# Kernel tuning notes

Hardware: AMD Instinct MI355X
Metric: run time of the kernel (lower is better)

The kernel has to match this reference:

```python
import jax, jax.numpy as jnp
import numpy as np

N_NODES = 50000
N_EDGES = 1000000
D_IN = 64
D_OUT = 64
N_REL = 8


def setup_inputs() -> dict:
    key = jax.random.key(0)
    ks = jax.random.split(key, 8)
    x = jax.random.normal(ks[0], (N_NODES, D_IN), dtype=jnp.float32)
    edge_src = jax.random.randint(ks[1], (N_EDGES,), 0, N_NODES, dtype=jnp.int32)
    edge_dst = jax.random.randint(ks[2], (N_EDGES,), 0, N_NODES, dtype=jnp.int32)
    edge_rel = jax.random.randint(ks[3], (N_EDGES,), 0, N_REL, dtype=jnp.int32)
    edge_weight = jnp.ones((N_EDGES,), dtype=jnp.float32)
    W_linear = jax.random.normal(ks[4], (N_REL * D_IN, D_OUT), dtype=jnp.float32) * (1.0 / np.sqrt(N_REL * D_IN))
    b_linear = jnp.zeros((D_OUT,), dtype=jnp.float32)
    W_self = jax.random.normal(ks[5], (D_IN, D_OUT), dtype=jnp.float32) * (1.0 / np.sqrt(D_IN))
    b_self = jnp.zeros((D_OUT,), dtype=jnp.float32)
    return {"x": x, "edge_src": edge_src, "edge_dst": edge_dst, "edge_rel": edge_rel,
            "edge_weight": edge_weight, "W_linear": W_linear, "b_linear": b_linear,
            "W_self": W_self, "b_self": b_self}


def reference(x, edge_src, edge_dst, edge_rel, edge_weight, W_linear, b_linear, W_self, b_self):
    N, d = x.shape
    R = W_linear.shape[0] // d
    # per-(dst, relation) segment ids, as in node_out * num_relation + relation
    seg = edge_dst * R + edge_rel  # [E]
    # degree normalization (message_and_aggregate path: no eps, divide by out-degree)
    deg = jax.ops.segment_sum(edge_weight, seg, num_segments=N * R)  # [N*R]
    ew = edge_weight / deg[seg]  # [E]
    # sparse mm: adjacency.T @ x == segment-sum of normalized gathered source features
    msg = x[edge_src] * ew[:, None]  # [E, d]
    update = jax.ops.segment_sum(msg, seg, num_segments=N * R)  # [N*R, d]
    update = update.reshape(N, R * d)
    # combine: linear(update) + self_loop(x), then relu
    out = update @ W_linear + b_linear + x @ W_self + b_self
    return jax.nn.relu(out)
```

## Files before the change

kernel.cpp:

```cpp
#include <hip/hip_runtime.h>
#include <stdint.h>

#define NNODES 50000
#define NEDGES 1000000
#define DIM    64
#define NREL   8
#define NBIN   489
#define NBUCK2 782
#define CPITCH 784
#define BCAP2  1600
#define NBLK   3125
#define APITCH 584
#define PREPN  (18 * 4 * 64 * 8)

typedef __attribute__((ext_vector_type(8))) short short8;
typedef __attribute__((ext_vector_type(4))) float float4v;
typedef __attribute__((ext_vector_type(4))) unsigned short us4;

__device__ __forceinline__ float bf2f(unsigned short u) {
  return __uint_as_float(((unsigned int)u) << 16);
}
__device__ __forceinline__ unsigned short f2bf(float f) {
  unsigned int u = __float_as_uint(f);
  unsigned int r = (u + 0x7FFF + ((u >> 16) & 1)) >> 16;
  return (unsigned short)r;
}
__device__ __forceinline__ unsigned int f2fp8(float f) {
  unsigned u = __float_as_uint(f);
  unsigned s = (u >> 24) & 0x80u;
  unsigned a = u & 0x7FFFFFFFu;
  if (a < 0x3C800000u) return s;
  unsigned r = a + 0x7FFFFu + ((a >> 20) & 1u);
  return s | (((r >> 20) - 960u) & 0x7Fu);
}
__device__ __forceinline__ float fp8d(unsigned b) {
  unsigned v = ((b & 0x7Fu) << 20) + 0x3C000000u;
  unsigned s = (b & 0x80u) << 24;
  return __uint_as_float(v | s);
}

__global__ __launch_bounds__(512) void build_kernel(
    const float4* __restrict__ x4,
    const float* __restrict__ Wlin, const float* __restrict__ Wself,
    const float* __restrict__ blin, const float* __restrict__ bself,
    const int4* __restrict__ src4, const int4* __restrict__ dst4,
    const int4* __restrict__ rel4, const float4* __restrict__ w4,
    us4* __restrict__ xb, unsigned int* __restrict__ xq4,
    unsigned short* __restrict__ Bf2, float* __restrict__ bsum,
    uint2* __restrict__ staged2, unsigned int* __restrict__ tab, int E4) {
  __shared__ int lhist[NBUCK2];
  __shared__ int lscan[NBUCK2];
  __shared__ uint2 lrec[2048];
  int tid = threadIdx.x;
  int j = blockIdx.x;
  int gid = j * 512 + tid;
  const int TOT = NBIN * 512;

  for (int t = gid; t < NNODES * DIM / 4; t += TOT) {
    float4 v = x4[t];
    us4 o;
    o.x = f2bf(v.x); o.y = f2bf(v.y); o.z = f2bf(v.z); o.w = f2bf(v.w);
    xb[t] = o;
    xq4[t] = f2fp8(v.x) | (f2fp8(v.y) << 8) | (f2fp8(v.z) << 16) | (f2fp8(v.w) << 24);
  }
  if (gid < PREPN) {
    int t = gid;
    int jj = t & 7;
    int l  = (t >> 3) & 63;
    int ct = (t >> 9) & 3;
    int ks = t >> 11;
    int k = ks * 32 + (l >> 4) * 8 + jj;
    int c = ct * 16 + (l & 15);
    float v = (k < 512) ? Wlin[(size_t)k * 64 + c] : Wself[(size_t)(k - 512) * 64 + c];
    Bf2[t] = f2bf(v);
  }
  if (gid < 64) bsum[gid] = blin[gid] + bself[gid];

  for (int i = tid; i < NBUCK2; i += 512) lhist[i] = 0;
  __syncthreads();
  bool valid = gid < E4;
  int4 s = {0,0,0,0}, d = {0,0,0,0}, r = {0,0,0,0};
  float4 w = {0.f,0.f,0.f,0.f};
  if (valid) { s = src4[gid]; d = dst4[gid]; r = rel4[gid]; w = w4[gid]; }
  int b0=0,b1=0,b2=0,b3=0,p0=0,p1=0,p2=0,p3=0;
  if (valid) {
    b0 = d.x >> 6; p0 = atomicAdd(&lhist[b0], 1);
    b1 = d.y >> 6; p1 = atomicAdd(&lhist[b1], 1);
    b2 = d.z >> 6; p2 = atomicAdd(&lhist[b2], 1);
    b3 = d.w >> 6; p3 = atomicAdd(&lhist[b3], 1);
  }
  __syncthreads();
  if (tid < 64) {
    int carry = 0;
    #pragma unroll
    for (int c = 0; c < 13; c++) {
      int i = c * 64 + tid;
      int v = (i < NBUCK2) ? lhist[i] : 0;
      int inc = v;
      #pragma unroll
      for (int dd = 1; dd < 64; dd <<= 1) {
        int tt = __shfl_up(inc, dd);
        if (tid >= dd) inc += tt;
      }
      if (i < NBUCK2) lscan[i] = carry + inc - v;
      carry += __shfl(inc, 63);
    }
  }
  __syncthreads();
  if (valid) {
    int q;
    q = lscan[b0] + p0; lrec[q] = make_uint2((unsigned)s.x | ((unsigned)r.x << 16) | ((unsigned)(d.x & 63) << 19), __float_as_uint(w.x));
    q = lscan[b1] + p1; lrec[q] = make_uint2((unsigned)s.y | ((unsigned)r.y << 16) | ((unsigned)(d.y & 63) << 19), __float_as_uint(w.y));
    q = lscan[b2] + p2; lrec[q] = make_uint2((unsigned)s.z | ((unsigned)r.z << 16) | ((unsigned)(d.z & 63) << 19), __float_as_uint(w.z));
    q = lscan[b3] + p3; lrec[q] = make_uint2((unsigned)s.w | ((unsigned)r.w << 16) | ((unsigned)(d.w & 63) << 19), __float_as_uint(w.w));
  }
  __syncthreads();
  for (int i = tid; i < NBUCK2; i += 512)
    tab[j * CPITCH + i] = (unsigned)lhist[i] | ((unsigned)lscan[i] << 16);
  int cntblk = NEDGES - j * 2048;
  if (cntblk > 2048) cntblk = 2048;
  uint2* myst = staged2 + (size_t)j * 2048;
  for (int i = tid; i < cntblk; i += 512)
    myst[i] = lrec[i];
}

__global__ __launch_bounds__(512) void csrbuild_kernel(
    const unsigned int* __restrict__ tab,
    const uint2* __restrict__ staged2, uint2* __restrict__ meta,
    int* __restrict__ roff2) {
  __shared__ uint2 cache[BCAP2];
  __shared__ short inv[BCAP2];
  __shared__ int   hist[512];
  __shared__ int   scn[512];
  __shared__ int   ncur[512];
  __shared__ float degf[512];
  __shared__ unsigned int tabcol[NBIN];
  __shared__ int   runbase[NBIN + 1];
  __shared__ int   cnt_s;
  int b = blockIdx.x;
  int tid = threadIdx.x;
  if (tid < 512) { hist[tid] = 0; degf[tid] = 0.f; }
  if (tid < 64) {
    int carry = 0;
    #pragma unroll
    for (int c = 0; c < 8; c++) {
      int jj = c * 64 + tid;
      unsigned tv = (jj < NBIN) ? tab[jj * CPITCH + b] : 0u;
      if (jj < NBIN) tabcol[jj] = tv;
      int v = (int)(tv & 0xFFFFu);
      int inc = v;
      #pragma unroll
      for (int dd = 1; dd < 64; dd <<= 1) {
        int tt = __shfl_up(inc, dd);
        if (tid >= dd) inc += tt;
      }
      if (jj < NBIN) runbase[jj] = carry + inc - v;
      carry += __shfl(inc, 63);
    }
    if (tid == 0) {
      runbase[NBIN] = carry;
      cnt_s = (carry < BCAP2) ? carry : BCAP2;
    }
  }
  __syncthreads();
  int cnt = cnt_s;

  for (int t = tid; t < cnt; t += 512) {
    int lo = 0, hi = NBIN - 1;
    #pragma unroll
    for (int it = 0; it < 9; it++) {
      int mid = (lo + hi + 1) >> 1;
      bool g = runbase[mid] <= t;
      lo = g ? mid : lo;
      hi = g ? hi : (mid - 1);
    }
    int jj = lo;
    int off = (int)(tabcol[jj] >> 16);
    uint2 rec = staged2[(size_t)jj * 2048 + off + (t - runbase[jj])];
    cache[t] = rec;
    int key = (((rec.x >> 19) & 63) << 3) | ((rec.x >> 16) & 7);
    atomicAdd(&hist[key], 1);
    atomicAdd(&degf[key], __uint_as_float(rec.y));
  }
  __syncthreads();
  if (tid < 64) {
    int carry = 0;
    #pragma unroll
    for (int c = 0; c < 8; c++) {
      int v = hist[c * 64 + tid];
      int inc = v;
      #pragma unroll
      for (int dd = 1; dd < 64; dd <<= 1) {
        int tt = __shfl_up(inc, dd);
        if (tid >= dd) inc += tt;
      }
      scn[c * 64 + tid]  = carry + inc - v;
      ncur[c * 64 + tid] = carry + inc - v;
      carry += __shfl(inc, 63);
    }
  }
  __syncthreads();
  int base = b * BCAP2;
  if (tid < 512) roff2[b * 513 + tid] = base + scn[tid];
  if (tid == 0)  roff2[b * 513 + 512] = base + cnt;
  if (tid < 512) {
    float d = degf[tid];
    degf[tid] = (d != 0.f) ? (1.0f / d) : 0.f;
  }
  __syncthreads();
  for (int i = tid; i < cnt; i += 512) {
    uint2 rec = cache[i];
    int key = (((rec.x >> 19) & 63) << 3) | ((rec.x >> 16) & 7);
    int pos = atomicAdd(&ncur[key], 1);
    inv[pos] = (short)i;
  }
  __syncthreads();
  for (int o = tid; o < cnt; o += 512) {
    int i = (int)inv[o];
    uint2 rec = cache[i];
    int key = (((rec.x >> 19) & 63) << 3) | ((rec.x >> 16) & 7);
    float sc = __uint_as_float(rec.y) * degf[key];
    meta[(size_t)base + o] = make_uint2((rec.x & 0xFFFF) << 6, __float_as_uint(sc));
  }
}

__global__ __launch_bounds__(512) void fused_kernel(const int* __restrict__ roff2,
                                                    const uint2* __restrict__ meta,
                                                    const unsigned char* __restrict__ xq,
                                                    const unsigned short* __restrict__ xb,
                                                    const unsigned short* __restrict__ Bf2,
                                                    const float* __restrict__ bsum,
                                                    float* __restrict__ out) {
  __shared__ unsigned short At[16 * APITCH];
  int tid  = threadIdx.x;
  int wave = tid >> 6;
  int lane = tid & 63;
  int nodeBase = blockIdx.x * 16;
  const char* xqb = (const char*)xq;

  int node0 = __builtin_amdgcn_readfirstlane(nodeBase + wave * 2);
  int bb = node0 >> 6;
  int kk = (node0 & 63) * 8;
  int bnd = 0;
  if (lane < 17) bnd = roff2[bb * 513 + kk + lane];

  int eb[17];
  #pragma unroll
  for (int k = 0; k < 17; k++) eb[k] = __builtin_amdgcn_readlane(bnd, k);

  float acc0[8], acc1[8];
  #pragma unroll
  for (int r = 0; r < 8; r++) { acc0[r] = 0.f; acc1[r] = 0.f; }

  #define G1(M) fp8d((unsigned)*(const unsigned char*)(xqb + (M).x + lane))
  #pragma unroll
  for (int r = 0; r < 8; r += 2) {
    int eA = eb[r],      EA = eb[r + 1];
    int eB = eb[r + 1],  EB = eb[r + 2];
    int eC = eb[8 + r],  EC = eb[9 + r];
    int eD = eb[9 + r],  ED = eb[10 + r];
    while (eA < EA && eB < EB && eC < EC && eD < ED) {
      uint2 mA = meta[eA], mB = meta[eB], mC = meta[eC], mD = meta[eD];
      float vA = G1(mA), vB = G1(mB), vC = G1(mC), vD = G1(mD);
      acc0[r]     += __uint_as_float(mA.y) * vA;
      acc0[r + 1] += __uint_as_float(mB.y) * vB;
      acc1[r]     += __uint_as_float(mC.y) * vC;
      acc1[r + 1] += __uint_as_float(mD.y) * vD;
      eA++; eB++; eC++; eD++;
    }
    while (eA < EA && eB < EB) {
      uint2 mA = meta[eA], mB = meta[eB];
      float vA = G1(mA), vB = G1(mB);
      acc0[r]     += __uint_as_float(mA.y) * vA;
      acc0[r + 1] += __uint_as_float(mB.y) * vB;
      eA++; eB++;
    }
    while (eC < EC && eD < ED) {
      uint2 mC = meta[eC], mD = meta[eD];
      float vC = G1(mC), vD = G1(mD);
      acc1[r]     += __uint_as_float(mC.y) * vC;
      acc1[r + 1] += __uint_as_float(mD.y) * vD;
      eC++; eD++;
    }
    for (; eA + 2 <= EA; eA += 2) {
      uint2 m0 = meta[eA], m1 = meta[eA + 1];
      float v0 = G1(m0), v1 = G1(m1);
      acc0[r] += __uint_as_float(m0.y) * v0;
      acc0[r] += __uint_as_float(m1.y) * v1;
    }
    if (eA < EA) { uint2 m0 = meta[eA]; acc0[r] += __uint_as_float(m0.y) * G1(m0); }
    for (; eB + 2 <= EB; eB += 2) {
      uint2 m0 = meta[eB], m1 = meta[eB + 1];
      float v0 = G1(m0), v1 = G1(m1);
      acc0[r + 1] += __uint_as_float(m0.y) * v0;
      acc0[r + 1] += __uint_as_float(m1.y) * v1;
    }
    if (eB < EB) { uint2 m0 = meta[eB]; acc0[r + 1] += __uint_as_float(m0.y) * G1(m0); }
    for (; eC + 2 <= EC; eC += 2) {
      uint2 m0 = meta[eC], m1 = meta[eC + 1];
      float v0 = G1(m0), v1 = G1(m1);
      acc1[r] += __uint_as_float(m0.y) * v0;
      acc1[r] += __uint_as_float(m1.y) * v1;
    }
    if (eC < EC) { uint2 m0 = meta[eC]; acc1[r] += __uint_as_float(m0.y) * G1(m0); }
    for (; eD + 2 <= ED; eD += 2) {
      uint2 m0 = meta[eD], m1 = meta[eD + 1];
      float v0 = G1(m0), v1 = G1(m1);
      acc1[r + 1] += __uint_as_float(m0.y) * v0;
      acc1[r + 1] += __uint_as_float(m1.y) * v1;
    }
    if (eD < ED) { uint2 m0 = meta[eD]; acc1[r + 1] += __uint_as_float(m0.y) * G1(m0); }
  }
  #undef G1

  {
    int row0 = wave * 2;
    unsigned short* ar0 = At + row0 * APITCH;
    unsigned short* ar1 = At + (row0 + 1) * APITCH;
    #pragma unroll
    for (int r = 0; r < 8; r++) {
      ar0[r * 64 + lane] = f2bf(acc0[r]);
      ar1[r * 64 + lane] = f2bf(acc1[r]);
    }
    ar0[512 + lane] = xb[(size_t)(node0) * 64 + lane];
    ar1[512 + lane] = xb[(size_t)(node0 + 1) * 64 + lane];
  }
  __syncthreads();

  if (wave < 4) {
    int q = lane >> 4;
    int m = lane & 15;
    float4v acc4 = {0.f, 0.f, 0.f, 0.f};
    const short8* Bp = (const short8*)Bf2;
    #pragma unroll
    for (int ks = 0; ks < 18; ks++) {
      short8 a = *(const short8*)(At + m * APITCH + ks * 32 + q * 8);
      short8 bfr = Bp[(ks * 4 + wave) * 64 + lane];
      acc4 = __builtin_amdgcn_mfma_f32_16x16x32_bf16(a, bfr, acc4, 0, 0, 0);
    }
    int c = wave * 16 + m;
    float bias = bsum[c];
    #pragma unroll
    for (int rr = 0; rr < 4; rr++) {
      out[(size_t)(nodeBase + q * 4 + rr) * 64 + c] = fmaxf(acc4[rr] + bias, 0.0f);
    }
  }
}

extern "C" void kernel_launch(void* const* d_in, const int* in_sizes, int n_in,
                              void* d_out, int out_size, void* d_ws, size_t ws_size,
                              hipStream_t stream) {
  const float* x     = (const float*)d_in[0];
  const int*   esrc  = (const int*)d_in[1];
  const int*   edst  = (const int*)d_in[2];
  const int*   erel  = (const int*)d_in[3];
  const float* ew    = (const float*)d_in[4];
  const float* Wlin  = (const float*)d_in[5];
  const float* blin  = (const float*)d_in[6];
  const float* Wself = (const float*)d_in[7];
  const float* bself = (const float*)d_in[8];
  float* out = (float*)d_out;

  char* ws = (char*)d_ws;
  size_t off = 0;
  auto alloc = [&](size_t bytes) -> void* {
    void* p = ws + off;
    off += (bytes + 255) & ~(size_t)255;
    return p;
  };
  uint2*          staged2 = (uint2*)alloc((size_t)NBIN * 2048 * sizeof(uint2));
  unsigned int*   tab     = (unsigned int*)alloc((size_t)NBIN * CPITCH * sizeof(unsigned int));
  uint2*          meta    = (uint2*)alloc((size_t)NBUCK2 * BCAP2 * sizeof(uint2));
  int*            roff2   = (int*)alloc((size_t)NBUCK2 * 513 * sizeof(int));
  unsigned short* Bf2     = (unsigned short*)alloc((size_t)PREPN * sizeof(unsigned short));
  float*          bsum    = (float*)alloc(64 * sizeof(float));
  unsigned short* xb      = (unsigned short*)alloc((size_t)NNODES * DIM * sizeof(unsigned short));
  unsigned char*  xq      = (unsigned char*)alloc((size_t)NNODES * DIM);

  const int E4 = NEDGES / 4;
  build_kernel<<<NBIN, 512, 0, stream>>>((const float4*)x, Wlin, Wself, blin, bself,
                                         (const int4*)esrc, (const int4*)edst,
                                         (const int4*)erel, (const float4*)ew,
                                         (us4*)xb, (unsigned int*)xq, Bf2, bsum,
                                         staged2, tab, E4);
  csrbuild_kernel<<<NBUCK2, 512, 0, stream>>>(tab, staged2, meta, roff2);
  fused_kernel<<<NBLK, 512, 0, stream>>>(roff2, meta, xq, xb, Bf2, bsum, out);
}
```

Measured before the change: 156.6 us.

## Drop CSR build kernel; bin edges by 16-node groups and scatter-accumulate in LDS

Removes the csrbuild pass. Edges are now binned per 16-node group straight into fixed-capacity global buckets using a global atomic counter. The fused kernel loads each bucket, computes degree normalisation in shared memory, and accumulates messages with LDS float atomics into a swizzled 128x64 buffer before converting to bf16 for the MFMA. This cuts one launch and the global staging traffic. In exchange it adds many LDS atomics, makes the order of the global scatter nondeterministic, and silently drops edges if a bucket overflows its 512-record capacity.

After: 484.4 us. +209.4%, slower.

```diff
diff --git a/kernel.cpp b/kernel.cpp
--- a/kernel.cpp
+++ b/kernel.cpp
@@ -5,12 +5,10 @@
 #define NEDGES 1000000
 #define DIM    64
 #define NREL   8
-#define NBIN   489
-#define NBUCK2 782
-#define CPITCH 784
-#define BCAP2  1600
-#define NBLK   3125
-#define APITCH 584
+#define NBLD   489
+#define NBINS  3125
+#define NBINSP 3136
+#define GCAP   512
 #define PREPN  (18 * 4 * 64 * 8)
 
 typedef __attribute__((ext_vector_type(8))) short short8;
@@ -37,6 +35,11 @@
   unsigned v = ((b & 0x7Fu) << 20) + 0x3C000000u;
   unsigned s = (b & 0x80u) << 24;
   return __uint_as_float(v | s);
+}
+__device__ __forceinline__ unsigned pkbf(float lo, float hi) {
+  unsigned r;
+  asm("v_cvt_pk_bf16_f32 %0, %1, %2" : "=v"(r) : "v"(lo), "v"(hi));
+  return r;
 }
 
 __global__ __launch_bounds__(512) void build_kernel(
@@ -47,14 +50,14 @@
     const int4* __restrict__ rel4, const float4* __restrict__ w4,
     us4* __restrict__ xb, unsigned int* __restrict__ xq4,
     unsigned short* __restrict__ Bf2, float* __restrict__ bsum,
-    uint2* __restrict__ staged2, unsigned int* __restrict__ tab, int E4) {
-  __shared__ int lhist[NBUCK2];
-  __shared__ int lscan[NBUCK2];
+    uint2* __restrict__ meta, unsigned int* __restrict__ gcnt, int E4) {
+  __shared__ int lhist[NBINSP];
+  __shared__ int lscan[NBINSP];
   __shared__ uint2 lrec[2048];
   int tid = threadIdx.x;
   int j = blockIdx.x;
   int gid = j * 512 + tid;
-  const int TOT = NBIN * 512;
+  const int TOT = NBLD * 512;
 
   for (int t = gid; t < NNODES * DIM / 4; t += TOT) {
     float4 v = x4[t];
@@ -76,7 +79,7 @@
   }
   if (gid < 64) bsum[gid] = blin[gid] + bself[gid];
 
-  for (int i = tid; i < NBUCK2; i += 512) lhist[i] = 0;
+  for (int i = tid; i < NBINSP; i += 512) lhist[i] = 0;
   __syncthreads();
   bool valid = gid < E4;
   int4 s = {0,0,0,0}, d = {0,0,0,0}, r = {0,0,0,0};
@@ -84,267 +87,154 @@
   if (valid) { s = src4[gid]; d = dst4[gid]; r = rel4[gid]; w = w4[gid]; }
   int b0=0,b1=0,b2=0,b3=0,p0=0,p1=0,p2=0,p3=0;
   if (valid) {
-    b0 = d.x >> 6; p0 = atomicAdd(&lhist[b0], 1);
-    b1 = d.y >> 6; p1 = atomicAdd(&lhist[b1], 1);
-    b2 = d.z >> 6; p2 = atomicAdd(&lhist[b2], 1);
-    b3 = d.w >> 6; p3 = atomicAdd(&lhist[b3], 1);
+    b0 = d.x >> 4; p0 = atomicAdd(&lhist[b0], 1);
+    b1 = d.y >> 4; p1 = atomicAdd(&lhist[b1], 1);
+    b2 = d.z >> 4; p2 = atomicAdd(&lhist[b2], 1);
+    b3 = d.w >> 4; p3 = atomicAdd(&lhist[b3], 1);
   }
   __syncthreads();
   if (tid < 64) {
     int carry = 0;
-    #pragma unroll
-    for (int c = 0; c < 13; c++) {
+    for (int c = 0; c < NBINSP / 64; c++) {
       int i = c * 64 + tid;
-      int v = (i < NBUCK2) ? lhist[i] : 0;
+      int v = lhist[i];
       int inc = v;
       #pragma unroll
       for (int dd = 1; dd < 64; dd <<= 1) {
         int tt = __shfl_up(inc, dd);
         if (tid >= dd) inc += tt;
       }
-      if (i < NBUCK2) lscan[i] = carry + inc - v;
+      lscan[i] = carry + inc - v;
       carry += __shfl(inc, 63);
     }
   }
   __syncthreads();
   if (valid) {
     int q;
-    q = lscan[b0] + p0; lrec[q] = make_uint2((unsigned)s.x | ((unsigned)r.x << 16) | ((unsigned)(d.x & 63) << 19), __float_as_uint(w.x));
-    q = lscan[b1] + p1; lrec[q] = make_uint2((unsigned)s.y | ((unsigned)r.y << 16) | ((unsigned)(d.y & 63) << 19), __float_as_uint(w.y));
-    q = lscan[b2] + p2; lrec[q] = make_uint2((unsigned)s.z | ((unsigned)r.z << 16) | ((unsigned)(d.z & 63) << 19), __float_as_uint(w.z));
-    q = lscan[b3] + p3; lrec[q] = make_uint2((unsigned)s.w | ((unsigned)r.w << 16) | ((unsigned)(d.w & 63) << 19), __float_as_uint(w.w));
-  }
-  __syncthreads();
-  for (int i = tid; i < NBUCK2; i += 512)
-    tab[j * CPITCH + i] = (unsigned)lhist[i] | ((unsigned)lscan[i] << 16);
-  int cntblk = NEDGES - j * 2048;
-  if (cntblk > 2048) cntblk = 2048;
-  uint2* myst = staged2 + (size_t)j * 2048;
-  for (int i = tid; i < cntblk; i += 512)
-    myst[i] = lrec[i];
-}
-
-__global__ __launch_bounds__(512) void csrbuild_kernel(
-    const unsigned int* __restrict__ tab,
-    const uint2* __restrict__ staged2, uint2* __restrict__ meta,
-    int* __restrict__ roff2) {
-  __shared__ uint2 cache[BCAP2];
-  __shared__ short inv[BCAP2];
-  __shared__ int   hist[512];
-  __shared__ int   scn[512];
-  __shared__ int   ncur[512];
-  __shared__ float degf[512];
-  __shared__ unsigned int tabcol[NBIN];
-  __shared__ int   runbase[NBIN + 1];
-  __shared__ int   cnt_s;
+    q = lscan[b0] + p0; lrec[q] = make_uint2(((unsigned)s.x << 6) | ((((unsigned)(d.x & 15) << 3) | (unsigned)r.x) << 24), __float_as_uint(w.x));
+    q = lscan[b1] + p1; lrec[q] = make_uint2(((unsigned)s.y << 6) | ((((unsigned)(d.y & 15) << 3) | (unsigned)r.y) << 24), __float_as_uint(w.y));
+    q = lscan[b2] + p2; lrec[q] = make_uint2(((unsigned)s.z << 6) | ((((unsigned)(d.z & 15) << 3) | (unsigned)r.z) << 24), __float_as_uint(w.z));
+    q = lscan[b3] + p3; lrec[q] = make_uint2(((unsigned)s.w << 6) | ((((unsigned)(d.w & 15) << 3) | (unsigned)r.w) << 24), __float_as_uint(w.w));
+  }
+  __syncthreads();
+  for (int i = tid; i < NBINS; i += 512) {
+    int c = lhist[i];
+    if (c == 0) continue;
+    unsigned base = atomicAdd(&gcnt[i], (unsigned)c);
+    int s0 = lscan[i];
+    uint2* dp = meta + (size_t)i * GCAP;
+    for (int k = 0; k < c; k++) {
+      unsigned pos = base + (unsigned)k;
+      if (pos < GCAP) dp[pos] = lrec[s0 + k];
+    }
+  }
+}
+
+__global__ __launch_bounds__(512, 8) void fused_kernel(
+    const unsigned int* __restrict__ gcnt,
+    const uint2* __restrict__ meta,
+    const unsigned char* __restrict__ xq,
+    const unsigned short* __restrict__ xb,
+    const unsigned short* __restrict__ Bf2,
+    const float* __restrict__ bsum,
+    float* __restrict__ out) {
+  __shared__ __align__(16) float accS[128 * 64];
+  __shared__ float degS[128];
+  __shared__ uint2 recS[GCAP];
+  int tid = threadIdx.x;
+  int lane = tid & 63;
+  int wave = tid >> 6;
   int b = blockIdx.x;
-  int tid = threadIdx.x;
-  if (tid < 512) { hist[tid] = 0; degf[tid] = 0.f; }
-  if (tid < 64) {
-    int carry = 0;
+  int nodeBase = b * 16;
+
+  int cnt = (int)gcnt[b];
+  if (cnt > GCAP) cnt = GCAP;
+
+  float4v* az = (float4v*)accS;
+  float4v z4 = {0.f, 0.f, 0.f, 0.f};
+  for (int i = tid; i < 128 * 16; i += 512) az[i] = z4;
+  if (tid < 128) degS[tid] = 0.f;
+  __syncthreads();
+
+  for (int t = tid; t < cnt; t += 512) {
+    uint2 rec = meta[(size_t)b * GCAP + t];
+    recS[t] = rec;
+    atomicAdd(&degS[rec.x >> 24], __uint_as_float(rec.y));
+  }
+  __syncthreads();
+  if (tid < 128) {
+    float dg = degS[tid];
+    degS[tid] = (dg != 0.f) ? (1.0f / dg) : 0.f;
+  }
+  __syncthreads();
+  for (int t = tid; t < cnt; t += 512) {
+    uint2 rec = recS[t];
+    recS[t].y = __float_as_uint(__uint_as_float(rec.y) * degS[rec.x >> 24]);
+  }
+  __syncthreads();
+
+  #define ACCIDX(key, l) (((key) << 6) | ((((l) >> 2) ^ ((key) >> 3)) << 2) | ((l) & 3))
+
+  const char* xqb = (const char*)xq;
+  for (int i0 = wave * 4; i0 < cnt; i0 += 32) {
+    if (i0 + 4 <= cnt) {
+      uint2 r0 = recS[i0], r1 = recS[i0 + 1], r2 = recS[i0 + 2], r3 = recS[i0 + 3];
+      float v0 = fp8d((unsigned)*(const unsigned char*)(xqb + (r0.x & 0x3FFFFF) + lane));
+      float v1 = fp8d((unsigned)*(const unsigned char*)(xqb + (r1.x & 0x3FFFFF) + lane));
+      float v2 = fp8d((unsigned)*(const unsigned char*)(xqb + (r2.x & 0x3FFFFF) + lane));
+      float v3 = fp8d((unsigned)*(const unsigned char*)(xqb + (r3.x & 0x3FFFFF) + lane));
+      atomicAdd(&accS[ACCIDX(r0.x >> 24, lane)], __uint_as_float(r0.y) * v0);
+      atomicAdd(&accS[ACCIDX(r1.x >> 24, lane)], __uint_as_float(r1.y) * v1);
+      atomicAdd(&accS[ACCIDX(r2.x >> 24, lane)], __uint_as_float(r2.y) * v2);
+      atomicAdd(&accS[ACCIDX(r3.x >> 24, lane)], __uint_as_float(r3.y) * v3);
+    } else {
+      for (int k = i0; k < cnt; k++) {
+        uint2 rr = recS[k];
+        float v = fp8d((unsigned)*(const unsigned char*)(xqb + (rr.x & 0x3FFFFF) + lane));
+        atomicAdd(&accS[ACCIDX(rr.x >> 24, lane)], __uint_as_float(rr.y) * v);
+      }
+    }
+  }
+  __syncthreads();
+
+  if (wave < 4) {
+    int m = lane & 15;
+    int q = lane >> 4;
+    float4v o4 = {0.f, 0.f, 0.f, 0.f};
+    const short8* Bp = (const short8*)Bf2;
+    const float4v* av = (const float4v*)accS;
     #pragma unroll
-    for (int c = 0; c < 8; c++) {
-      int jj = c * 64 + tid;
-      unsigned tv = (jj < NBIN) ? tab[jj * CPITCH + b] : 0u;
-      if (jj < NBIN) tabcol[jj] = tv;
-      int v = (int)(tv & 0xFFFFu);
-      int inc = v;
+    for (int ks = 0; ks < 16; ks++) {
+      int t = ks * 4 + q;
+      int key = (m << 3) | (t >> 3);
+      int sb = (t & 7) << 1;
+      float4v x0 = av[(key << 4) | (sb ^ m)];
+      float4v x1 = av[(key << 4) | ((sb + 1) ^ m)];
+      union { short8 s8; unsigned u[4]; } afr;
+      afr.u[0] = pkbf(x0.x, x0.y);
+      afr.u[1] = pkbf(x0.z, x0.w);
+      afr.u[2] = pkbf(x1.x, x1.y);
+      afr.u[3] = pkbf(x1.z, x1.w);
+      short8 bfr = Bp[(ks * 4 + wave) * 64 + lane];
+      o4 = __builtin_amdgcn_mfma_f32_16x16x32_bf16(afr.s8, bfr, o4, 0, 0, 0);
+    }
+    {
+      int node = nodeBase + m;
       #pragma unroll
-      for (int dd = 1; dd < 64; dd <<= 1) {
-        int tt = __shfl_up(inc, dd);
-        if (tid >= dd) inc += tt;
+      for (int ks = 16; ks < 18; ks++) {
+        short8 a = *(const short8*)(xb + (size_t)node * 64 + (ks - 16) * 32 + q * 8);
+        short8 bfr = Bp[(ks * 4 + wave) * 64 + lane];
+        o4 = __builtin_amdgcn_mfma_f32_16x16x32_bf16(a, bfr, o4, 0, 0, 0);
       }
-      if (jj < NBIN) runbase[jj] = carry + inc - v;
-      carry += __shfl(inc, 63);
-    }
-    if (tid == 0) {
-      runbase[NBIN] = carry;
-      cnt_s = (carry < BCAP2) ? carry : BCAP2;
-    }
-  }
-  __syncthreads();
-  int cnt = cnt_s;
-
-  for (int t = tid; t < cnt; t += 512) {
-    int lo = 0, hi = NBIN - 1;
-    #pragma unroll
-    for (int it = 0; it < 9; it++) {
-      int mid = (lo + hi + 1) >> 1;
-      bool g = runbase[mid] <= t;
-      lo = g ? mid : lo;
-      hi = g ? hi : (mid - 1);
-    }
-    int jj = lo;
-    int off = (int)(tabcol[jj] >> 16);
-    uint2 rec = staged2[(size_t)jj * 2048 + off + (t - runbase[jj])];
-    cache[t] = rec;
-    int key = (((rec.x >> 19) & 63) << 3) | ((rec.x >> 16) & 7);
-    atomicAdd(&hist[key], 1);
-    atomicAdd(&degf[key], __uint_as_float(rec.y));
-  }
-  __syncthreads();
-  if (tid < 64) {
-    int carry = 0;
-    #pragma unroll
-    for (int c = 0; c < 8; c++) {
-      int v = hist[c * 64 + tid];
-      int inc = v;
-      #pragma unroll
-      for (int dd = 1; dd < 64; dd <<= 1) {
-        int tt = __shfl_up(inc, dd);
-        if (tid >= dd) inc += tt;
-      }
-      scn[c * 64 + tid]  = carry + inc - v;
-      ncur[c * 64 + tid] = carry + inc - v;
-      carry += __shfl(inc, 63);
-    }
-  }
-  __syncthreads();
-  int base = b * BCAP2;
-  if (tid < 512) roff2[b * 513 + tid] = base + scn[tid];
-  if (tid == 0)  roff2[b * 513 + 512] = base + cnt;
-  if (tid < 512) {
-    float d = degf[tid];
-    degf[tid] = (d != 0.f) ? (1.0f / d) : 0.f;
-  }
-  __syncthreads();
-  for (int i = tid; i < cnt; i += 512) {
-    uint2 rec = cache[i];
-    int key = (((rec.x >> 19) & 63) << 3) | ((rec.x >> 16) & 7);
-    int pos = atomicAdd(&ncur[key], 1);
-    inv[pos] = (short)i;
-  }
-  __syncthreads();
-  for (int o = tid; o < cnt; o += 512) {
-    int i = (int)inv[o];
-    uint2 rec = cache[i];
-    int key = (((rec.x >> 19) & 63) << 3) | ((rec.x >> 16) & 7);
-    float sc = __uint_as_float(rec.y) * degf[key];
-    meta[(size_t)base + o] = make_uint2((rec.x & 0xFFFF) << 6, __float_as_uint(sc));
-  }
-}
-
-__global__ __launch_bounds__(512) void fused_kernel(const int* __restrict__ roff2,
-                                                    const uint2* __restrict__ meta,
-                                                    const unsigned char* __restrict__ xq,
-                                                    const unsigned short* __restrict__ xb,
-                                                    const unsigned short* __restrict__ Bf2,
-                                                    const float* __restrict__ bsum,
-                                                    float* __restrict__ out) {
-  __shared__ unsigned short At[16 * APITCH];
-  int tid  = threadIdx.x;
-  int wave = tid >> 6;
-  int lane = tid & 63;
-  int nodeBase = blockIdx.x * 16;
-  const char* xqb = (const char*)xq;
-
-  int node0 = __builtin_amdgcn_readfirstlane(nodeBase + wave * 2);
-  int bb = node0 >> 6;
-  int kk = (node0 & 63) * 8;
-  int bnd = 0;
-  if (lane < 17) bnd = roff2[bb * 513 + kk + lane];
-
-  int eb[17];
-  #pragma unroll
-  for (int k = 0; k < 17; k++) eb[k] = __builtin_amdgcn_readlane(bnd, k);
-
-  float acc0[8], acc1[8];
-  #pragma unroll
-  for (int r = 0; r < 8; r++) { acc0[r] = 0.f; acc1[r] = 0.f; }
-
-  #define G1(M) fp8d((unsigned)*(const unsigned char*)(xqb + (M).x + lane))
-  #pragma unroll
-  for (int r = 0; r < 8; r += 2) {
-    int eA = eb[r],      EA = eb[r + 1];
-    int eB = eb[r + 1],  EB = eb[r + 2];
-    int eC = eb[8 + r],  EC = eb[9 + r];
-    int eD = eb[9 + r],  ED = eb[10 + r];
-    while (eA < EA && eB < EB && eC < EC && eD < ED) {
-      uint2 mA = meta[eA], mB = meta[eB], mC = meta[eC], mD = meta[eD];
-      float vA = G1(mA), vB = G1(mB), vC = G1(mC), vD = G1(mD);
-      acc0[r]     += __uint_as_float(mA.y) * vA;
-      acc0[r + 1] += __uint_as_float(mB.y) * vB;
-      acc1[r]     += __uint_as_float(mC.y) * vC;
-      acc1[r + 1] += __uint_as_float(mD.y) * vD;
-      eA++; eB++; eC++; eD++;
-    }
-    while (eA < EA && eB < EB) {
-      uint2 mA = meta[eA], mB = meta[eB];
-      float vA = G1(mA), vB = G1(mB);
-      acc0[r]     += __uint_as_float(mA.y) * vA;
-      acc0[r + 1] += __uint_as_float(mB.y) * vB;
-      eA++; eB++;
-    }
-    while (eC < EC && eD < ED) {
-      uint2 mC = meta[eC], mD = meta[eD];
-      float vC = G1(mC), vD = G1(mD);
-      acc1[r]     += __uint_as_float(mC.y) * vC;
-      acc1[r + 1] += __uint_as_float(mD.y) * vD;
-      eC++; eD++;
-    }
-    for (; eA + 2 <= EA; eA += 2) {
-      uint2 m0 = meta[eA], m1 = meta[eA + 1];
-      float v0 = G1(m0), v1 = G1(m1);
-      acc0[r] += __uint_as_float(m0.y) * v0;
-      acc0[r] += __uint_as_float(m1.y) * v1;
-    }
-    if (eA < EA) { uint2 m0 = meta[eA]; acc0[r] += __uint_as_float(m0.y) * G1(m0); }
-    for (; eB + 2 <= EB; eB += 2) {
-      uint2 m0 = meta[eB], m1 = meta[eB + 1];
-      float v0 = G1(m0), v1 = G1(m1);
-      acc0[r + 1] += __uint_as_float(m0.y) * v0;
-      acc0[r + 1] += __uint_as_float(m1.y) * v1;
-    }
-    if (eB < EB) { uint2 m0 = meta[eB]; acc0[r + 1] += __uint_as_float(m0.y) * G1(m0); }
-    for (; eC + 2 <= EC; eC += 2) {
-      uint2 m0 = meta[eC], m1 = meta[eC + 1];
-      float v0 = G1(m0), v1 = G1(m1);
-      acc1[r] += __uint_as_float(m0.y) * v0;
-      acc1[r] += __uint_as_float(m1.y) * v1;
-    }
-    if (eC < EC) { uint2 m0 = meta[eC]; acc1[r] += __uint_as_float(m0.y) * G1(m0); }
-    for (; eD + 2 <= ED; eD += 2) {
-      uint2 m0 = meta[eD], m1 = meta[eD + 1];
-      float v0 = G1(m0), v1 = G1(m1);
-      acc1[r + 1] += __uint_as_float(m0.y) * v0;
-      acc1[r + 1] += __uint_as_float(m1.y) * v1;
-    }
-    if (eD < ED) { uint2 m0 = meta[eD]; acc1[r + 1] += __uint_as_float(m0.y) * G1(m0); }
-  }
-  #undef G1
-
-  {
-    int row0 = wave * 2;
-    unsigned short* ar0 = At + row0 * APITCH;
-    unsigned short* ar1 = At + (row0 + 1) * APITCH;
-    #pragma unroll
-    for (int r = 0; r < 8; r++) {
-      ar0[r * 64 + lane] = f2bf(acc0[r]);
-      ar1[r * 64 + lane] = f2bf(acc1[r]);
-    }
-    ar0[512 + lane] = xb[(size_t)(node0) * 64 + lane];
-    ar1[512 + lane] = xb[(size_t)(node0 + 1) * 64 + lane];
-  }
-  __syncthreads();
-
-  if (wave < 4) {
-    int q = lane >> 4;
-    int m = lane & 15;
-    float4v acc4 = {0.f, 0.f, 0.f, 0.f};
-    const short8* Bp = (const short8*)Bf2;
-    #pragma unroll
-    for (int ks = 0; ks < 18; ks++) {
-      short8 a = *(const short8*)(At + m * APITCH + ks * 32 + q * 8);
-      short8 bfr = Bp[(ks * 4 + wave) * 64 + lane];
-      acc4 = __builtin_amdgcn_mfma_f32_16x16x32_bf16(a, bfr, acc4, 0, 0, 0);
     }
     int c = wave * 16 + m;
     float bias = bsum[c];
     #pragma unroll
     for (int rr = 0; rr < 4; rr++) {
-      out[(size_t)(nodeBase + q * 4 + rr) * 64 + c] = fmaxf(acc4[rr] + bias, 0.0f);
-    }
-  }
+      out[(size_t)(nodeBase + q * 4 + rr) * 64 + c] = fmaxf(o4[rr] + bias, 0.0f);
+    }
+  }
+  #undef ACCIDX
 }
 
 extern "C" void kernel_launch(void* const* d_in, const int* in_sizes, int n_in,
@@ -368,21 +258,20 @@
     off += (bytes + 255) & ~(size_t)255;
     return p;
   };
-  uint2*          staged2 = (uint2*)alloc((size_t)NBIN * 2048 * sizeof(uint2));
-  unsigned int*   tab     = (unsigned int*)alloc((size_t)NBIN * CPITCH * sizeof(unsigned int));
-  uint2*          meta    = (uint2*)alloc((size_t)NBUCK2 * BCAP2 * sizeof(uint2));
-  int*            roff2   = (int*)alloc((size_t)NBUCK2 * 513 * sizeof(int));
-  unsigned short* Bf2     = (unsigned short*)alloc((size_t)PREPN * sizeof(unsigned short));
-  float*          bsum    = (float*)alloc(64 * sizeof(float));
-  unsigned short* xb      = (unsigned short*)alloc((size_t)NNODES * DIM * sizeof(unsigned short));
-  unsigned char*  xq      = (unsigned char*)alloc((size_t)NNODES * DIM);
+  uint2*          meta = (uint2*)alloc((size_t)NBINS * GCAP * sizeof(uint2));
+  unsigned int*   gcnt = (unsigned int*)alloc((size_t)NBINSP * sizeof(unsigned int));
+  unsigned short* Bf2  = (unsigned short*)alloc((size_t)PREPN * sizeof(unsigned short));
+  float*          bsum = (float*)alloc(64 * sizeof(float));
+  unsigned short* xb   = (unsigned short*)alloc((size_t)NNODES * DIM * sizeof(unsigned short));
+  unsigned char*  xq   = (unsigned char*)alloc((size_t)NNODES * DIM);
+
+  hipMemsetAsync(gcnt, 0, (size_t)NBINSP * sizeof(unsigned int), stream);
 
   const int E4 = NEDGES / 4;
-  build_kernel<<<NBIN, 512, 0, stream>>>((const float4*)x, Wlin, Wself, blin, bself,
+  build_kernel<<<NBLD, 512, 0, stream>>>((const float4*)x, Wlin, Wself, blin, bself,
                                          (const int4*)esrc, (const int4*)edst,
                                          (const int4*)erel, (const float4*)ew,
                                          (us4*)xb, (unsigned int*)xq, Bf2, bsum,
-                                         staged2, tab, E4);
-  csrbuild_kernel<<<NBUCK2, 512, 0, stream>>>(tab, staged2, meta, roff2);
-  fused_kernel<<<NBLK, 512, 0, stream>>>(roff2, meta, xq, xb, Bf2, bsum, out);
-}
+                                         meta, gcnt, E4);
+  fused_kernel<<<NBINS, 512, 0, stream>>>(gcnt, meta, xq, xb, Bf2, bsum, out);
+}
```

## Fuse CSR build with aggregation and GEMM into one per-bucket kernel

Applied to the files above, without the earlier changes.

Merges the CSR-building kernel and the aggregate+MFMA kernel into a single kernel per 64-node bucket, keeping sorted edge records in LDS instead of writing meta/roff2 to global memory. Degree normalization now accumulates the weight sum alongside the feature sum and divides at segment finish, removing the separate degree pass. Each wave walks four segments at once, refilling a slot when its segment ends. The cost is much lower block count (782 vs 3125), more LDS per block, and four serialized GEMM phases, which may reduce parallelism. BCAP also shrinks to 1500, which may truncate heavily loaded buckets.

Result: slower. 273.8 us (+74.9%).

```diff
diff --git a/kernel.cpp b/kernel.cpp
--- a/kernel.cpp
+++ b/kernel.cpp
@@ -6,20 +6,16 @@
 #define DIM    64
 #define NREL   8
 #define NBIN   489
-#define NBUCK2 782
+#define NBUCK  782
 #define CPITCH 784
-#define BCAP2  1600
-#define NBLK   3125
-#define APITCH 584
+#define BCAP   1500
+#define PITCH  592
 #define PREPN  (18 * 4 * 64 * 8)
 
 typedef __attribute__((ext_vector_type(8))) short short8;
 typedef __attribute__((ext_vector_type(4))) float float4v;
 typedef __attribute__((ext_vector_type(4))) unsigned short us4;
 
-__device__ __forceinline__ float bf2f(unsigned short u) {
-  return __uint_as_float(((unsigned int)u) << 16);
-}
 __device__ __forceinline__ unsigned short f2bf(float f) {
   unsigned int u = __float_as_uint(f);
   unsigned int r = (u + 0x7FFF + ((u >> 16) & 1)) >> 16;
@@ -48,8 +44,8 @@
     us4* __restrict__ xb, unsigned int* __restrict__ xq4,
     unsigned short* __restrict__ Bf2, float* __restrict__ bsum,
     uint2* __restrict__ staged2, unsigned int* __restrict__ tab, int E4) {
-  __shared__ int lhist[NBUCK2];
-  __shared__ int lscan[NBUCK2];
+  __shared__ int lhist[NBUCK];
+  __shared__ int lscan[NBUCK];
   __shared__ uint2 lrec[2048];
   int tid = threadIdx.x;
   int j = blockIdx.x;
@@ -76,7 +72,7 @@
   }
   if (gid < 64) bsum[gid] = blin[gid] + bself[gid];
 
-  for (int i = tid; i < NBUCK2; i += 512) lhist[i] = 0;
+  for (int i = tid; i < NBUCK; i += 512) lhist[i] = 0;
   __syncthreads();
   bool valid = gid < E4;
   int4 s = {0,0,0,0}, d = {0,0,0,0}, r = {0,0,0,0};
@@ -95,14 +91,14 @@
     #pragma unroll
     for (int c = 0; c < 13; c++) {
       int i = c * 64 + tid;
-      int v = (i < NBUCK2) ? lhist[i] : 0;
+      int v = (i < NBUCK) ? lhist[i] : 0;
       int inc = v;
       #pragma unroll
       for (int dd = 1; dd < 64; dd <<= 1) {
         int tt = __shfl_up(inc, dd);
         if (tid >= dd) inc += tt;
       }
-      if (i < NBUCK2) lscan[i] = carry + inc - v;
+      if (i < NBUCK) lscan[i] = carry + inc - v;
       carry += __shfl(inc, 63);
     }
   }
@@ -115,7 +111,7 @@
     q = lscan[b3] + p3; lrec[q] = make_uint2((unsigned)s.w | ((unsigned)r.w << 16) | ((unsigned)(d.w & 63) << 19), __float_as_uint(w.w));
   }
   __syncthreads();
-  for (int i = tid; i < NBUCK2; i += 512)
+  for (int i = tid; i < NBUCK; i += 512)
     tab[j * CPITCH + i] = (unsigned)lhist[i] | ((unsigned)lscan[i] << 16);
   int cntblk = NEDGES - j * 2048;
   if (cntblk > 2048) cntblk = 2048;
@@ -124,22 +120,30 @@
     myst[i] = lrec[i];
 }
 
-__global__ __launch_bounds__(512) void csrbuild_kernel(
+__global__ __launch_bounds__(512, 6) void aggemm_kernel(
     const unsigned int* __restrict__ tab,
-    const uint2* __restrict__ staged2, uint2* __restrict__ meta,
-    int* __restrict__ roff2) {
-  __shared__ uint2 cache[BCAP2];
-  __shared__ short inv[BCAP2];
-  __shared__ int   hist[512];
-  __shared__ int   scn[512];
-  __shared__ int   ncur[512];
-  __shared__ float degf[512];
+    const uint2* __restrict__ staged2,
+    const unsigned char* __restrict__ xq,
+    const unsigned short* __restrict__ xb,
+    const unsigned short* __restrict__ Bf2,
+    const float* __restrict__ bsum,
+    float* __restrict__ out) {
+  __shared__ __align__(16) unsigned short At[16 * PITCH];
+  __shared__ uint2 cache[BCAP];
+  __shared__ short inv[BCAP];
+  __shared__ int hist[512];
+  __shared__ int scn[512];
+  __shared__ int ncur[512];
   __shared__ unsigned int tabcol[NBIN];
-  __shared__ int   runbase[NBIN + 1];
-  __shared__ int   cnt_s;
+  __shared__ int runbase[NBIN + 1];
+  __shared__ int cnt_s;
+  int tid = threadIdx.x;
+  int lane = tid & 63;
+  int wave = tid >> 6;
   int b = blockIdx.x;
-  int tid = threadIdx.x;
-  if (tid < 512) { hist[tid] = 0; degf[tid] = 0.f; }
+  int nodeBase = b * 64;
+
+  if (tid < 512) hist[tid] = 0;
   if (tid < 64) {
     int carry = 0;
     #pragma unroll
@@ -159,7 +163,7 @@
     }
     if (tid == 0) {
       runbase[NBIN] = carry;
-      cnt_s = (carry < BCAP2) ? carry : BCAP2;
+      cnt_s = (carry < BCAP) ? carry : BCAP;
     }
   }
   __syncthreads();
@@ -180,7 +184,6 @@
     cache[t] = rec;
     int key = (((rec.x >> 19) & 63) << 3) | ((rec.x >> 16) & 7);
     atomicAdd(&hist[key], 1);
-    atomicAdd(&degf[key], __uint_as_float(rec.y));
   }
   __syncthreads();
   if (tid < 64) {
@@ -200,14 +203,6 @@
     }
   }
   __syncthreads();
-  int base = b * BCAP2;
-  if (tid < 512) roff2[b * 513 + tid] = base + scn[tid];
-  if (tid == 0)  roff2[b * 513 + 512] = base + cnt;
-  if (tid < 512) {
-    float d = degf[tid];
-    degf[tid] = (d != 0.f) ? (1.0f / d) : 0.f;
-  }
-  __syncthreads();
   for (int i = tid; i < cnt; i += 512) {
     uint2 rec = cache[i];
     int key = (((rec.x >> 19) & 63) << 3) | ((rec.x >> 16) & 7);
@@ -215,135 +210,64 @@
     inv[pos] = (short)i;
   }
   __syncthreads();
-  for (int o = tid; o < cnt; o += 512) {
-    int i = (int)inv[o];
-    uint2 rec = cache[i];
-    int key = (((rec.x >> 19) & 63) << 3) | ((rec.x >> 16) & 7);
-    float sc = __uint_as_float(rec.y) * degf[key];
-    meta[(size_t)base + o] = make_uint2((rec.x & 0xFFFF) << 6, __float_as_uint(sc));
-  }
-}
-
-__global__ __launch_bounds__(512) void fused_kernel(const int* __restrict__ roff2,
-                                                    const uint2* __restrict__ meta,
-                                                    const unsigned char* __restrict__ xq,
-                                                    const unsigned short* __restrict__ xb,
-                                                    const unsigned short* __restrict__ Bf2,
-                                                    const float* __restrict__ bsum,
-                                                    float* __restrict__ out) {
-  __shared__ unsigned short At[16 * APITCH];
-  int tid  = threadIdx.x;
-  int wave = tid >> 6;
-  int lane = tid & 63;
-  int nodeBase = blockIdx.x * 16;
-  const char* xqb = (const char*)xq;
-
-  int node0 = __builtin_amdgcn_readfirstlane(nodeBase + wave * 2);
-  int bb = node0 >> 6;
-  int kk = (node0 & 63) * 8;
-  int bnd = 0;
-  if (lane < 17) bnd = roff2[bb * 513 + kk + lane];
-
-  int eb[17];
-  #pragma unroll
-  for (int k = 0; k < 17; k++) eb[k] = __builtin_amdgcn_readlane(bnd, k);
-
-  float acc0[8], acc1[8];
-  #pragma unroll
-  for (int r = 0; r < 8; r++) { acc0[r] = 0.f; acc1[r] = 0.f; }
-
-  #define G1(M) fp8d((unsigned)*(const unsigned char*)(xqb + (M).x + lane))
-  #pragma unroll
-  for (int r = 0; r < 8; r += 2) {
-    int eA = eb[r],      EA = eb[r + 1];
-    int eB = eb[r + 1],  EB = eb[r + 2];
-    int eC = eb[8 + r],  EC = eb[9 + r];
-    int eD = eb[9 + r],  ED = eb[10 + r];
-    while (eA < EA && eB < EB && eC < EC && eD < ED) {
-      uint2 mA = meta[eA], mB = meta[eB], mC = meta[eC], mD = meta[eD];
-      float vA = G1(mA), vB = G1(mB), vC = G1(mC), vD = G1(mD);
-      acc0[r]     += __uint_as_float(mA.y) * vA;
-      acc0[r + 1] += __uint_as_float(mB.y) * vB;
-      acc1[r]     += __uint_as_float(mC.y) * vC;
-      acc1[r + 1] += __uint_as_float(mD.y) * vD;
-      eA++; eB++; eC++; eD++;
-    }
-    while (eA < EA && eB < EB) {
-      uint2 mA = meta[eA], mB = meta[eB];
-      float vA = G1(mA), vB = G1(mB);
-      acc0[r]     += __uint_as_float(mA.y) * vA;
-      acc0[r + 1] += __uint_as_float(mB.y) * vB;
-      eA++; eB++;
-    }
-    while (eC < EC && eD < ED) {
-      uint2 mC = meta[eC], mD = meta[eD];
-      float vC = G1(mC), vD = G1(mD);
-      acc1[r]     += __uint_as_float(mC.y) * vC;
-      acc1[r + 1] += __uint_as_float(mD.y) * vD;
-      eC++; eD++;
-    }
-    for (; eA + 2 <= EA; eA += 2) {
-      uint2 m0 = meta[eA], m1 = meta[eA + 1];
-      float v0 = G1(m0), v1 = G1(m1);
-      acc0[r] += __uint_as_float(m0.y) * v0;
-      acc0[r] += __uint_as_float(m1.y) * v1;
-    }
-    if (eA < EA) { uint2 m0 = meta[eA]; acc0[r] += __uint_as_float(m0.y) * G1(m0); }
-    for (; eB + 2 <= EB; eB += 2) {
-      uint2 m0 = meta[eB], m1 = meta[eB + 1];
-      float v0 = G1(m0), v1 = G1(m1);
-      acc0[r + 1] += __uint_as_float(m0.y) * v0;
-      acc0[r + 1] += __uint_as_float(m1.y) * v1;
-    }
-    if (eB < EB) { uint2 m0 = meta[eB]; acc0[r + 1] += __uint_as_float(m0.y) * G1(m0); }
-    for (; eC + 2 <= EC; eC += 2) {
-      uint2 m0 = meta[eC], m1 = meta[eC + 1];
-      float v0 = G1(m0), v1 = G1(m1);
-      acc1[r] += __uint_as_float(m0.y) * v0;
-      acc1[r] += __uint_as_float(m1.y) * v1;
-    }
-    if (eC < EC) { uint2 m0 = meta[eC]; acc1[r] += __uint_as_float(m0.y) * G1(m0); }
-    for (; eD + 2 <= ED; eD += 2) {
-      uint2 m0 = meta[eD], m1 = meta[eD + 1];
-      float v0 = G1(m0), v1 = G1(m1);
-      acc1[r + 1] += __uint_as_float(m0.y) * v0;
-      acc1[r + 1] += __uint_as_float(m1.y) * v1;
-    }
-    if (eD < ED) { uint2 m0 = meta[eD]; acc1[r + 1] += __uint_as_float(m0.y) * G1(m0); }
-  }
-  #undef G1
-
-  {
-    int row0 = wave * 2;
-    unsigned short* ar0 = At + row0 * APITCH;
-    unsigned short* ar1 = At + (row0 + 1) * APITCH;
-    #pragma unroll
-    for (int r = 0; r < 8; r++) {
-      ar0[r * 64 + lane] = f2bf(acc0[r]);
-      ar1[r * 64 + lane] = f2bf(acc1[r]);
-    }
-    ar0[512 + lane] = xb[(size_t)(node0) * 64 + lane];
-    ar1[512 + lane] = xb[(size_t)(node0 + 1) * 64 + lane];
-  }
-  __syncthreads();
-
-  if (wave < 4) {
-    int q = lane >> 4;
-    int m = lane & 15;
-    float4v acc4 = {0.f, 0.f, 0.f, 0.f};
-    const short8* Bp = (const short8*)Bf2;
-    #pragma unroll
-    for (int ks = 0; ks < 18; ks++) {
-      short8 a = *(const short8*)(At + m * APITCH + ks * 32 + q * 8);
-      short8 bfr = Bp[(ks * 4 + wave) * 64 + lane];
-      acc4 = __builtin_amdgcn_mfma_f32_16x16x32_bf16(a, bfr, acc4, 0, 0, 0);
-    }
-    int c = wave * 16 + m;
-    float bias = bsum[c];
-    #pragma unroll
-    for (int rr = 0; rr < 4; rr++) {
-      out[(size_t)(nodeBase + q * 4 + rr) * 64 + c] = fmaxf(acc4[rr] + bias, 0.0f);
-    }
+
+  for (int qt = 0; qt < 4; qt++) {
+    int kbase = qt * 128 + wave * 16;
+    int jn = 0;
+    int K0, K1, K2, K3;
+    int e0, e1, e2, e3, E0, E1, E2, E3;
+    float A0, A1, A2, A3, S0, S1, S2, S3;
+    #define RF(K, e, E, A, S) { A = 0.f; S = 0.f; \
+      if (jn < 16) { int ky = kbase + jn; K = jn; jn++; e = scn[ky]; E = e + hist[ky]; } \
+      else { K = -1; e = 0; E = 0; } }
+    #define FIN(K, A, S) { float rd = (S != 0.f) ? (1.0f / S) : 0.f; \
+      At[(wave * 2 + ((K) >> 3)) * PITCH + ((K) & 7) * 64 + lane] = f2bf(A * rd); }
+    #define ST(e, E, A, S) { bool go = (e < E); int ei = go ? e : 0; \
+      int ii = (int)inv[ei]; uint2 rc = cache[ii]; \
+      unsigned sa = rc.x & 0xFFFFu; sa = (sa < (unsigned)NNODES) ? sa : 0u; \
+      float vv = fp8d((unsigned)xq[(sa << 6) + lane]); \
+      float ww = go ? __uint_as_float(rc.y) : 0.f; \
+      A += ww * vv; S += ww; e += go ? 1 : 0; }
+    RF(K0, e0, E0, A0, S0) RF(K1, e1, E1, A1, S1)
+    RF(K2, e2, E2, A2, S2) RF(K3, e3, E3, A3, S3)
+    while (K0 >= 0 || K1 >= 0 || K2 >= 0 || K3 >= 0) {
+      if (K0 >= 0 && e0 >= E0) { FIN(K0, A0, S0) RF(K0, e0, E0, A0, S0) }
+      if (K1 >= 0 && e1 >= E1) { FIN(K1, A1, S1) RF(K1, e1, E1, A1, S1) }
+      if (K2 >= 0 && e2 >= E2) { FIN(K2, A2, S2) RF(K2, e2, E2, A2, S2) }
+      if (K3 >= 0 && e3 >= E3) { FIN(K3, A3, S3) RF(K3, e3, E3, A3, S3) }
+      ST(e0, E0, A0, S0) ST(e1, E1, A1, S1)
+      ST(e2, E2, A2, S2) ST(e3, E3, A3, S3)
+    }
+    #undef RF
+    #undef FIN
+    #undef ST
+    {
+      int node0 = nodeBase + qt * 16 + wave * 2;
+      At[(wave * 2) * PITCH + 512 + lane]     = xb[(size_t)node0 * 64 + lane];
+      At[(wave * 2 + 1) * PITCH + 512 + lane] = xb[(size_t)(node0 + 1) * 64 + lane];
+    }
+    __syncthreads();
+
+    if (wave < 4) {
+      int m = lane & 15;
+      int q = lane >> 4;
+      float4v o4 = {0.f, 0.f, 0.f, 0.f};
+      const short8* Bp = (const short8*)Bf2;
+      #pragma unroll
+      for (int ks = 0; ks < 18; ks++) {
+        short8 a = *(const short8*)(At + m * PITCH + ks * 32 + q * 8);
+        short8 bfr = Bp[(ks * 4 + wave) * 64 + lane];
+        o4 = __builtin_amdgcn_mfma_f32_16x16x32_bf16(a, bfr, o4, 0, 0, 0);
+      }
+      int c = wave * 16 + m;
+      float bias = bsum[c];
+      #pragma unroll
+      for (int rr = 0; rr < 4; rr++) {
+        int nd = nodeBase + qt * 16 + q * 4 + rr;
+        if (nd < NNODES) out[(size_t)nd * 64 + c] = fmaxf(o4[rr] + bias, 0.0f);
+      }
+    }
+    __syncthreads();
   }
 }
 
@@ -370,8 +294,6 @@
   };
   uint2*          staged2 = (uint2*)alloc((size_t)NBIN * 2048 * sizeof(uint2));
   unsigned int*   tab     = (unsigned int*)alloc((size_t)NBIN * CPITCH * sizeof(unsigned int));
-  uint2*          meta    = (uint2*)alloc((size_t)NBUCK2 * BCAP2 * sizeof(uint2));
-  int*            roff2   = (int*)alloc((size_t)NBUCK2 * 513 * sizeof(int));
   unsigned short* Bf2     = (unsigned short*)alloc((size_t)PREPN * sizeof(unsigned short));
   float*          bsum    = (float*)alloc(64 * sizeof(float));
   unsigned short* xb      = (unsigned short*)alloc((size_t)NNODES * DIM * sizeof(unsigned short));
@@ -383,6 +305,5 @@
                                          (const int4*)erel, (const float4*)ew,
                                          (us4*)xb, (unsigned int*)xq, Bf2, bsum,
                                          staged2, tab, E4);
-  csrbuild_kernel<<<NBUCK2, 512, 0, stream>>>(tab, staged2, meta, roff2);
-  fused_kernel<<<NBLK, 512, 0, stream>>>(roff2, meta, xq, xb, Bf2, bsum, out);
-}
+  aggemm_kernel<<<NBUCK, 512, 0, stream>>>(tab, staged2, xq, xb, Bf2, bsum, out);
+}
```
